# Kernel optimization log

Hardware: AMD Instinct MI355X
Metric: run time of the kernel (lower is better)

The kernel has to match this reference:

```python
import jax, jax.numpy as jnp
import numpy as np

N_NODES = 100000
N_EDGES = 1600000
IN_DIM, HID_DIM, OUT_DIM = 128, 32, 32


def setup_inputs() -> dict:
    key = jax.random.key(0)
    k1, k2, k3, k4, k5 = jax.random.split(key, 5)
    x = jax.random.normal(k1, (N_NODES, IN_DIM), dtype=jnp.float32)
    W1 = jax.random.normal(k2, (IN_DIM, HID_DIM), dtype=jnp.float32) * (1.0 / np.sqrt(IN_DIM))
    W2 = jax.random.normal(k3, (HID_DIM, OUT_DIM), dtype=jnp.float32) * (1.0 / np.sqrt(HID_DIM))
    edge_weight = jax.random.uniform(k4, (N_EDGES,), dtype=jnp.float32)
    edge_index = jax.random.randint(k5, (2, N_EDGES), 0, N_NODES, dtype=jnp.int64)
    return {"x": x, "W1": W1, "W2": W2, "edge_weight": edge_weight, "edge_index": edge_index}


def _gcn_conv(x, W, edge_index, edge_weight):
    # GCNConv with add_self_loops=False, normalize=False, bias=False:
    # h = x @ W ; out[dst] += edge_weight * h[src]
    src, dst = edge_index[0], edge_index[1]
    h = x @ W                                   # [N, out]
    msg = h[src] * edge_weight[:, None]         # [E, out] gather + scale
    return jax.ops.segment_sum(msg, dst, num_segments=x.shape[0])  # scatter-add


def reference(x, W1, W2, edge_weight, edge_index):
    h = _gcn_conv(x, W1, edge_index, edge_weight)   # no activation in source
    z = _gcn_conv(h, W2, edge_index, edge_weight)
    return z
```

## Files before the change

kernel.cpp:

```cpp
#include <hip/hip_runtime.h>

#define N_NODES 100000
#define N_EDGES 1600000
#define IN_DIM 128
#define HID_DIM 32

#define NPB 256
#define BSHIFT 8
#define NBUCK ((N_NODES + NPB - 1) / NPB)
#define EPB 4096
#define NBLK_E ((N_EDGES + EPB - 1) / EPB)
#define OSTRIDE (NBUCK + 1)
#define CAPB 4608
#define MMROWS 128
#define NBLK_MM ((N_NODES + MMROWS - 1) / MMROWS)
#define XS_STRIDE 136

typedef __attribute__((ext_vector_type(8))) short bf16x8;
typedef __attribute__((ext_vector_type(4))) float f32x4;

__device__ __forceinline__ unsigned int pack_bf16x2(float a0, float a1) {
    unsigned int u0 = __float_as_uint(a0), u1 = __float_as_uint(a1);
    u0 = (u0 + 0x7FFFu + ((u0 >> 16) & 1u)) >> 16;
    u1 = (u1 + 0x7FFFu + ((u1 >> 16) & 1u)) >> 16;
    return u0 | (u1 << 16);
}

__device__ __forceinline__ unsigned short bf16_of(float v) {
    unsigned int u = __float_as_uint(v);
    u = (u + 0x7FFFu + ((u >> 16) & 1u)) >> 16;
    return (unsigned short)u;
}

__device__ __forceinline__ int scan512(int v, int* wtmp) {
    const int t = threadIdx.x, lane = t & 63, wv = t >> 6;
    int incl = v;
#pragma unroll
    for (int o = 1; o < 64; o <<= 1) {
        const int n = __shfl_up(incl, o, 64);
        if (lane >= o) incl += n;
    }
    if (lane == 63) wtmp[wv] = incl;
    __syncthreads();
    if (t < 8) {
        const int wval = wtmp[t];
        int s = wval;
#pragma unroll
        for (int o = 1; o < 8; o <<= 1) {
            const int n = __shfl_up(s, o, 64);
            if (t >= o) s += n;
        }
        wtmp[t] = s - wval;
    }
    __syncthreads();
    return incl + wtmp[wv];
}

__global__ __launch_bounds__(512) void fusedA(const int* __restrict__ ei,
                                              const float* __restrict__ ew,
                                              int* __restrict__ bcnt,
                                              int2* __restrict__ pairAlin,
                                              int* __restrict__ ostart,
                                              const float* __restrict__ x,
                                              const float* __restrict__ W,
                                              unsigned int* __restrict__ h) {
    __shared__ __align__(16) char smem[36000];
    const int tid = threadIdx.x;

    if (blockIdx.x < NBLK_E) {
        int2* stag   = (int2*)smem;
        int*  lh     = (int*)(smem + 32768);
        int*  lstart = (int*)(smem + 34336);
        int*  wtmp   = (int*)(smem + 35904);

        for (int j = tid; j < NBUCK; j += 512) lh[j] = 0;
        __syncthreads();

        const int e0 = blockIdx.x * EPB;
        int dstr[8];
#pragma unroll
        for (int u = 0; u < 8; ++u) {
            const int e = e0 + u * 512 + tid;
            dstr[u] = (e < N_EDGES) ? ei[N_EDGES + e] : -1;
            if (dstr[u] >= 0) atomicAdd(&lh[dstr[u] >> BSHIFT], 1);
        }
        __syncthreads();

        const int v = (tid < NBUCK) ? lh[tid] : 0;
        const int incl = scan512(v, wtmp);
        if (tid < NBUCK) {
            lstart[tid] = incl - v;
            if (v) atomicAdd(&bcnt[tid], v);
        }
        if (tid == NBUCK - 1) lstart[NBUCK] = incl;
        __syncthreads();
        if (tid < NBUCK) lh[tid] = 0;
        __syncthreads();

#pragma unroll
        for (int u = 0; u < 8; ++u) {
            const int e = e0 + u * 512 + tid;
            const int d = dstr[u];
            if (d >= 0) {
                const int b = d >> BSHIFT;
                const int slot = atomicAdd(&lh[b], 1);
                stag[lstart[b] + slot] =
                    make_int2(ei[e] | ((d & (NPB - 1)) << 17), __float_as_int(ew[e]));
            }
        }
        __syncthreads();

        const int total = lstart[NBUCK];
        for (int i = tid; i < total; i += 512)
            pairAlin[(size_t)blockIdx.x * EPB + i] = stag[i];
        if (tid < OSTRIDE) ostart[blockIdx.x * OSTRIDE + tid] = lstart[tid];
    } else {
        unsigned short* xbf = (unsigned short*)smem;
        const int lane = tid & 63, w = tid >> 6;
        const int row0 = (blockIdx.x - NBLK_E) * MMROWS;

#pragma unroll
        for (int i = 0; i < 8; ++i) {
            const int idx = tid + i * 512;
            const int r = idx >> 5, c4 = idx & 31;
            const int grow = row0 + r;
            float4 vv = (grow < N_NODES) ? ((const float4*)x)[(size_t)grow * 32 + c4]
                                         : make_float4(0.f, 0.f, 0.f, 0.f);
            *(uint2*)&xbf[r * XS_STRIDE + c4 * 4] =
                make_uint2(pack_bf16x2(vv.x, vv.y), pack_bf16x2(vv.z, vv.w));
        }

        const int colB = lane & 15, kg = lane >> 4;
        bf16x8 bfrag[2][4];
#pragma unroll
        for (int n = 0; n < 2; ++n)
#pragma unroll
            for (int kt = 0; kt < 4; ++kt) {
                const int kbase = kt * 32 + kg * 8;
                bf16x8 f;
#pragma unroll
                for (int j = 0; j < 8; ++j)
                    f[j] = (short)bf16_of(W[(size_t)(kbase + j) * HID_DIM + n * 16 + colB]);
                bfrag[n][kt] = f;
            }
        __syncthreads();

        f32x4 acc0 = {0.f, 0.f, 0.f, 0.f}, acc1 = {0.f, 0.f, 0.f, 0.f};
        const int arow = w * 16 + (lane & 15);
#pragma unroll
        for (int kt = 0; kt < 4; ++kt) {
            bf16x8 a = *(bf16x8*)&xbf[arow * XS_STRIDE + kt * 32 + kg * 8];
            acc0 = __builtin_amdgcn_mfma_f32_16x16x32_bf16(a, bfrag[0][kt], acc0, 0, 0, 0);
            acc1 = __builtin_amdgcn_mfma_f32_16x16x32_bf16(a, bfrag[1][kt], acc1, 0, 0, 0);
        }
        __syncthreads();

        float* cst = (float*)smem;
        float* cw_ = cst + w * 576;
        const int crow = (lane >> 4) * 4;
#pragma unroll
        for (int r = 0; r < 4; ++r) {
            cw_[(crow + r) * 36 + (lane & 15)] = acc0[r];
            cw_[(crow + r) * 36 + 16 + (lane & 15)] = acc1[r];
        }
        __syncthreads();
        const int r = tid >> 2, q = tid & 3;
        const int grow = row0 + r;
        if (grow < N_NODES) {
            const float* cr = cst + (r >> 4) * 576 + (r & 15) * 36 + q * 8;
            uint4 o = make_uint4(pack_bf16x2(cr[0], cr[1]), pack_bf16x2(cr[2], cr[3]),
                                 pack_bf16x2(cr[4], cr[5]), pack_bf16x2(cr[6], cr[7]));
            ((uint4*)h)[(size_t)grow * 4 + q] = o;
        }
    }
}

__global__ __launch_bounds__(512) void phaseB(const int* __restrict__ bcnt,
                                              const int* __restrict__ ostart,
                                              const int2* __restrict__ pairAlin,
                                              unsigned int* __restrict__ csr,
                                              int* __restrict__ offs) {
    __shared__ int2 stag[CAPB];
    __shared__ unsigned int stag2[CAPB];
    __shared__ int st[NBLK_E];
    __shared__ int P[NBLK_E + 1];
    __shared__ int lh[NPB];
    __shared__ int wtmp[8];
    const int b = blockIdx.x;
    const int t = threadIdx.x;

    int* red = (int*)stag2;
    red[t] = (t < b) ? bcnt[t] : 0;
    __syncthreads();
    for (int s = 256; s > 0; s >>= 1) {
        if (t < s) red[t] += red[t + s];
        __syncthreads();
    }
    const int base_out = red[0];
    __syncthreads();

    int len = 0;
    if (t < NBLK_E) {
        const int s0 = ostart[t * OSTRIDE + b];
        st[t] = s0;
        len = ostart[t * OSTRIDE + b + 1] - s0;
    }
    const int incl = scan512(len, wtmp);
    if (t < NBLK_E) P[t] = incl - len;
    if (t == NBLK_E - 1) P[NBLK_E] = incl;
    __syncthreads();
    const int cnt = min(P[NBLK_E], CAPB);

    for (int i = t; i < cnt; i += 512) {
        int lo = 0, hi = NBLK_E - 1;
        while (lo < hi) {
            const int mid = (lo + hi + 1) >> 1;
            if (P[mid] <= i) lo = mid; else hi = mid - 1;
        }
        stag[i] = pairAlin[(size_t)lo * EPB + st[lo] + (i - P[lo])];
    }
    if (t < NPB) lh[t] = 0;
    __syncthreads();

    for (int i = t; i < cnt; i += 512)
        atomicAdd(&lh[(stag[i].x >> 17) & (NPB - 1)], 1);
    __syncthreads();

    const int v = (t < NPB) ? lh[t] : 0;
    const int incl2 = scan512(v, wtmp);
    if (t < NPB) {
        const int excl = incl2 - v;
        lh[t] = excl;
        const int node = (b << BSHIFT) + t;
        if (node < N_NODES) offs[node] = base_out + excl;
    }
    if (b == NBUCK - 1 && t == 0) offs[N_NODES] = base_out + cnt;
    __syncthreads();

    for (int i = t; i < cnt; i += 512) {
        const int2 p = stag[i];
        const int dl = (p.x >> 17) & (NPB - 1);
        const int pos = atomicAdd(&lh[dl], 1);
        const unsigned int wb = bf16_of(__int_as_float(p.y));
        stag2[pos] = (unsigned int)(p.x & 0x1FFFF) | ((wb & 0x7FFFu) << 17);
    }
    __syncthreads();
    for (int i = t; i < cnt; i += 512) csr[base_out + i] = stag2[i];
}


__device__ __forceinline__ void bf16fma8(float acc[8], const uint4 v, const float w) {
    acc[0] += w * __uint_as_float(v.x << 16);
    acc[1] += w * __uint_as_float(v.x & 0xFFFF0000u);
    acc[2] += w * __uint_as_float(v.y << 16);
    acc[3] += w * __uint_as_float(v.y & 0xFFFF0000u);
    acc[4] += w * __uint_as_float(v.z << 16);
    acc[5] += w * __uint_as_float(v.z & 0xFFFF0000u);
    acc[6] += w * __uint_as_float(v.w << 16);
    acc[7] += w * __uint_as_float(v.w & 0xFFFF0000u);
}

__device__ __forceinline__ void edge_accum(const int* __restrict__ offs,
                                           const unsigned int* __restrict__ csr,
                                           const uint4* __restrict__ h,
                                           int node, int ln, float acc[8]) {
    int i = offs[node];
    const int end = offs[node + 1];
    for (; i + 3 < end; i += 4) {
        const unsigned int e0 = csr[i], e1 = csr[i + 1], e2 = csr[i + 2], e3 = csr[i + 3];
        const uint4 v0 = h[(size_t)(e0 & 0x1FFFF) * 4 + ln];
        const uint4 v1 = h[(size_t)(e1 & 0x1FFFF) * 4 + ln];
        const uint4 v2 = h[(size_t)(e2 & 0x1FFFF) * 4 + ln];
        const uint4 v3 = h[(size_t)(e3 & 0x1FFFF) * 4 + ln];
        bf16fma8(acc, v0, __uint_as_float((e0 >> 17) << 16));
        bf16fma8(acc, v1, __uint_as_float((e1 >> 17) << 16));
        bf16fma8(acc, v2, __uint_as_float((e2 >> 17) << 16));
        bf16fma8(acc, v3, __uint_as_float((e3 >> 17) << 16));
    }
    for (; i < end; ++i) {
        const unsigned int e = csr[i];
        bf16fma8(acc, h[(size_t)(e & 0x1FFFF) * 4 + ln], __uint_as_float((e >> 17) << 16));
    }
}

__global__ __launch_bounds__(256) void gather_mm(const int* __restrict__ offs,
                                                 const unsigned int* __restrict__ csr,
                                                 const uint4* __restrict__ h1,
                                                 const float* __restrict__ W2,
                                                 uint4* __restrict__ h2) {
    __shared__ float W2s[HID_DIM * HID_DIM];
    __shared__ float a1s[64 * 33];
    const int tid = threadIdx.x;
    ((float4*)W2s)[tid] = ((const float4*)W2)[tid];
    const int g = tid >> 2, ln = tid & 3;
    const int node = blockIdx.x * 64 + g;
    const int node_c = min(node, N_NODES - 1);

    float acc[8] = {0.f, 0.f, 0.f, 0.f, 0.f, 0.f, 0.f, 0.f};
    edge_accum(offs, csr, h1, node_c, ln, acc);

    __syncthreads();
#pragma unroll
    for (int j = 0; j < 8; ++j) a1s[g * 33 + 8 * ln + j] = acc[j];
    __syncthreads();

    const float* ar = a1s + g * 33;
    float s[8] = {0.f, 0.f, 0.f, 0.f, 0.f, 0.f, 0.f, 0.f};
#pragma unroll
    for (int k = 0; k < HID_DIM; ++k) {
        const float av = ar[k];
        const float* wr = W2s + k * HID_DIM + 8 * ln;
#pragma unroll
        for (int j = 0; j < 8; ++j) s[j] += av * wr[j];
    }
    if (node < N_NODES)
        h2[(size_t)node * 4 + ln] = make_uint4(pack_bf16x2(s[0], s[1]),
                                               pack_bf16x2(s[2], s[3]),
                                               pack_bf16x2(s[4], s[5]),
                                               pack_bf16x2(s[6], s[7]));
}

__global__ __launch_bounds__(256) void gather_out(const int* __restrict__ offs,
                                                  const unsigned int* __restrict__ csr,
                                                  const uint4* __restrict__ h2,
                                                  float* __restrict__ out) {
    const int tid = threadIdx.x;
    const int g = tid >> 2, ln = tid & 3;
    const int node = blockIdx.x * 64 + g;
    if (node >= N_NODES) return;

    float acc[8] = {0.f, 0.f, 0.f, 0.f, 0.f, 0.f, 0.f, 0.f};
    edge_accum(offs, csr, h2, node, ln, acc);
    ((float4*)out)[(size_t)node * 8 + 2 * ln] = make_float4(acc[0], acc[1], acc[2], acc[3]);
    ((float4*)out)[(size_t)node * 8 + 2 * ln + 1] = make_float4(acc[4], acc[5], acc[6], acc[7]);
}

extern "C" void kernel_launch(void* const* d_in, const int* in_sizes, int n_in,
                              void* d_out, int out_size, void* d_ws, size_t ws_size,
                              hipStream_t stream) {
    const float* x  = (const float*)d_in[0];
    const float* W1 = (const float*)d_in[1];
    const float* W2 = (const float*)d_in[2];
    const float* ew = (const float*)d_in[3];
    const int*   ei = (const int*)d_in[4];
    float* out = (float*)d_out;

    int2* pairAlin = (int2*)d_ws;
    unsigned int* csr = (unsigned int*)(pairAlin + (size_t)NBLK_E * EPB);
    unsigned int* h1u = csr + N_EDGES;
    unsigned int* h2u = h1u + (size_t)N_NODES * 16;
    int*  offs   = (int*)(h2u + (size_t)N_NODES * 16);
    int*  bcnt   = offs + N_NODES + 1;
    int*  ostart = bcnt + NBUCK;

    hipMemsetAsync(bcnt, 0, NBUCK * sizeof(int), stream);
    fusedA<<<NBLK_E + NBLK_MM, 512, 0, stream>>>(ei, ew, bcnt, pairAlin, ostart,
                                                 x, W1, h1u);

    phaseB<<<NBUCK, 512, 0, stream>>>(bcnt, ostart, pairAlin, csr, offs);

    gather_mm<<<(N_NODES + 63) / 64, 256, 0, stream>>>(offs, csr, (const uint4*)h1u,
                                                       W2, (uint4*)h2u);

    gather_out<<<(N_NODES + 63) / 64, 256, 0, stream>>>(offs, csr, (const uint4*)h2u, out);
}
```

Measured before the change: 104.1 us.

## Split edge staging into SoA with bf16 weights and unroll gather by eight

The intermediate edge buffer changes from int2 pairs into separate arrays: a uint32 holding the source index plus local destination, and a uint16 bf16 weight. This cuts the workspace traffic written by fusedA and read by phaseB from 8 to 6 bytes per edge, and lowers LDS use in both kernels. The CSR gather loop is also unrolled to 8 edges with a 4-edge remainder step, so more independent h-row loads are in flight. The cost is more registers per thread in the gather kernels and the bf16 weight rounding happening earlier, which gives the same result as before.

```diff
diff --git a/kernel.cpp b/kernel.cpp
--- a/kernel.cpp
+++ b/kernel.cpp
@@ -59,7 +59,8 @@
 __global__ __launch_bounds__(512) void fusedA(const int* __restrict__ ei,
                                               const float* __restrict__ ew,
                                               int* __restrict__ bcnt,
-                                              int2* __restrict__ pairAlin,
+                                              unsigned int* __restrict__ ulin,
+                                              unsigned short* __restrict__ wlin,
                                               int* __restrict__ ostart,
                                               const float* __restrict__ x,
                                               const float* __restrict__ W,
@@ -68,10 +69,11 @@
     const int tid = threadIdx.x;
 
     if (blockIdx.x < NBLK_E) {
-        int2* stag   = (int2*)smem;
-        int*  lh     = (int*)(smem + 32768);
-        int*  lstart = (int*)(smem + 34336);
-        int*  wtmp   = (int*)(smem + 35904);
+        unsigned int*   stag_u = (unsigned int*)smem;
+        unsigned short* stag_w = (unsigned short*)(smem + 16384);
+        int* lh     = (int*)(smem + 24576);
+        int* lstart = (int*)(smem + 26144);
+        int* wtmp   = (int*)(smem + 27712);
 
         for (int j = tid; j < NBUCK; j += 512) lh[j] = 0;
         __syncthreads();
@@ -104,15 +106,19 @@
             if (d >= 0) {
                 const int b = d >> BSHIFT;
                 const int slot = atomicAdd(&lh[b], 1);
-                stag[lstart[b] + slot] =
-                    make_int2(ei[e] | ((d & (NPB - 1)) << 17), __float_as_int(ew[e]));
+                const int p = lstart[b] + slot;
+                stag_u[p] = (unsigned int)ei[e] | ((unsigned int)(d & (NPB - 1)) << 17);
+                stag_w[p] = bf16_of(ew[e]);
             }
         }
         __syncthreads();
 
         const int total = lstart[NBUCK];
-        for (int i = tid; i < total; i += 512)
-            pairAlin[(size_t)blockIdx.x * EPB + i] = stag[i];
+        const size_t gbase = (size_t)blockIdx.x * EPB;
+        for (int i = tid; i < total; i += 512) {
+            ulin[gbase + i] = stag_u[i];
+            wlin[gbase + i] = stag_w[i];
+        }
         if (tid < OSTRIDE) ostart[blockIdx.x * OSTRIDE + tid] = lstart[tid];
     } else {
         unsigned short* xbf = (unsigned short*)smem;
@@ -177,11 +183,13 @@
 
 __global__ __launch_bounds__(512) void phaseB(const int* __restrict__ bcnt,
                                               const int* __restrict__ ostart,
-                                              const int2* __restrict__ pairAlin,
+                                              const unsigned int* __restrict__ ulin,
+                                              const unsigned short* __restrict__ wlin,
                                               unsigned int* __restrict__ csr,
                                               int* __restrict__ offs) {
-    __shared__ int2 stag[CAPB];
-    __shared__ unsigned int stag2[CAPB];
+    __shared__ unsigned int   stag_u[CAPB];
+    __shared__ unsigned short stag_w[CAPB];
+    __shared__ unsigned int   stag2[CAPB];
     __shared__ int st[NBLK_E];
     __shared__ int P[NBLK_E + 1];
     __shared__ int lh[NPB];
@@ -217,13 +225,15 @@
             const int mid = (lo + hi + 1) >> 1;
             if (P[mid] <= i) lo = mid; else hi = mid - 1;
         }
-        stag[i] = pairAlin[(size_t)lo * EPB + st[lo] + (i - P[lo])];
+        const size_t g = (size_t)lo * EPB + st[lo] + (i - P[lo]);
+        stag_u[i] = ulin[g];
+        stag_w[i] = wlin[g];
     }
     if (t < NPB) lh[t] = 0;
     __syncthreads();
 
     for (int i = t; i < cnt; i += 512)
-        atomicAdd(&lh[(stag[i].x >> 17) & (NPB - 1)], 1);
+        atomicAdd(&lh[(stag_u[i] >> 17) & (NPB - 1)], 1);
     __syncthreads();
 
     const int v = (t < NPB) ? lh[t] : 0;
@@ -238,11 +248,10 @@
     __syncthreads();
 
     for (int i = t; i < cnt; i += 512) {
-        const int2 p = stag[i];
-        const int dl = (p.x >> 17) & (NPB - 1);
+        const unsigned int u = stag_u[i];
+        const int dl = (u >> 17) & (NPB - 1);
         const int pos = atomicAdd(&lh[dl], 1);
-        const unsigned int wb = bf16_of(__int_as_float(p.y));
-        stag2[pos] = (unsigned int)(p.x & 0x1FFFF) | ((wb & 0x7FFFu) << 17);
+        stag2[pos] = (u & 0x1FFFF) | ((unsigned int)(stag_w[i] & 0x7FFFu) << 17);
     }
     __syncthreads();
     for (int i = t; i < cnt; i += 512) csr[base_out + i] = stag2[i];
@@ -266,16 +275,28 @@
                                            int node, int ln, float acc[8]) {
     int i = offs[node];
     const int end = offs[node + 1];
-    for (; i + 3 < end; i += 4) {
-        const unsigned int e0 = csr[i], e1 = csr[i + 1], e2 = csr[i + 2], e3 = csr[i + 3];
-        const uint4 v0 = h[(size_t)(e0 & 0x1FFFF) * 4 + ln];
-        const uint4 v1 = h[(size_t)(e1 & 0x1FFFF) * 4 + ln];
-        const uint4 v2 = h[(size_t)(e2 & 0x1FFFF) * 4 + ln];
-        const uint4 v3 = h[(size_t)(e3 & 0x1FFFF) * 4 + ln];
-        bf16fma8(acc, v0, __uint_as_float((e0 >> 17) << 16));
-        bf16fma8(acc, v1, __uint_as_float((e1 >> 17) << 16));
-        bf16fma8(acc, v2, __uint_as_float((e2 >> 17) << 16));
-        bf16fma8(acc, v3, __uint_as_float((e3 >> 17) << 16));
+    for (; i + 7 < end; i += 8) {
+        unsigned int e[8];
+        uint4 v[8];
+#pragma unroll
+        for (int j = 0; j < 8; ++j) e[j] = csr[i + j];
+#pragma unroll
+        for (int j = 0; j < 8; ++j) v[j] = h[(size_t)(e[j] & 0x1FFFF) * 4 + ln];
+#pragma unroll
+        for (int j = 0; j < 8; ++j)
+            bf16fma8(acc, v[j], __uint_as_float((e[j] >> 17) << 16));
+    }
+    if (i + 3 < end) {
+        unsigned int e[4];
+        uint4 v[4];
+#pragma unroll
+        for (int j = 0; j < 4; ++j) e[j] = csr[i + j];
+#pragma unroll
+        for (int j = 0; j < 4; ++j) v[j] = h[(size_t)(e[j] & 0x1FFFF) * 4 + ln];
+#pragma unroll
+        for (int j = 0; j < 4; ++j)
+            bf16fma8(acc, v[j], __uint_as_float((e[j] >> 17) << 16));
+        i += 4;
     }
     for (; i < end; ++i) {
         const unsigned int e = csr[i];
@@ -345,19 +366,20 @@
     const int*   ei = (const int*)d_in[4];
     float* out = (float*)d_out;
 
-    int2* pairAlin = (int2*)d_ws;
-    unsigned int* csr = (unsigned int*)(pairAlin + (size_t)NBLK_E * EPB);
-    unsigned int* h1u = csr + N_EDGES;
-    unsigned int* h2u = h1u + (size_t)N_NODES * 16;
+    unsigned int*   ulin = (unsigned int*)d_ws;
+    unsigned short* wlin = (unsigned short*)(ulin + N_EDGES);
+    unsigned int*   csr  = (unsigned int*)(wlin + N_EDGES);
+    unsigned int*   h1u  = csr + N_EDGES;
+    unsigned int*   h2u  = h1u + (size_t)N_NODES * 16;
     int*  offs   = (int*)(h2u + (size_t)N_NODES * 16);
     int*  bcnt   = offs + N_NODES + 1;
     int*  ostart = bcnt + NBUCK;
 
     hipMemsetAsync(bcnt, 0, NBUCK * sizeof(int), stream);
-    fusedA<<<NBLK_E + NBLK_MM, 512, 0, stream>>>(ei, ew, bcnt, pairAlin, ostart,
+    fusedA<<<NBLK_E + NBLK_MM, 512, 0, stream>>>(ei, ew, bcnt, ulin, wlin, ostart,
                                                  x, W1, h1u);
 
-    phaseB<<<NBUCK, 512, 0, stream>>>(bcnt, ostart, pairAlin, csr, offs);
+    phaseB<<<NBUCK, 512, 0, stream>>>(bcnt, ostart, ulin, wlin, csr, offs);
 
     gather_mm<<<(N_NODES + 63) / 64, 256, 0, stream>>>(offs, csr, (const uint4*)h1u,
                                                        W2, (uint4*)h2u);
```

After: 103.9 us. About the same (-0.2%).
